# Kernel tuning notes

Measured on AMD Instinct MI355X. Metric: run time of the kernel, lower is better.

Reference implementation:

```python
import jax, jax.numpy as jnp
import numpy as np

GRID_SIZE = 5
SPLINE_ORDER = 3
NUM_BASIS = GRID_SIZE + SPLINE_ORDER  # 8
GRID = jnp.linspace(-1.0, 1.0, GRID_SIZE + 2 * SPLINE_ORDER + 1)  # [12]
EPS = 1e-6


def bspline_basis(x):
    """Iterative Cox-de Boor. x: [...]; returns [..., NUM_BASIS]."""
    xe = x[..., None]
    # order-0 indicator basis: [..., G-1]
    B = ((xe >= GRID[:-1]) & (xe < GRID[1:])).astype(x.dtype)
    for k in range(1, SPLINE_ORDER + 1):
        nb = B.shape[-1] - 1
        g_i = GRID[:nb]
        g_i1 = GRID[1:1 + nb]
        g_ik = GRID[k:k + nb]
        g_ik1 = GRID[k + 1:k + 1 + nb]
        dl = g_ik - g_i
        dr = g_ik1 - g_i1
        left = jnp.where(dl > EPS, (xe - g_i) / jnp.where(dl > EPS, dl, 1.0), 0.0) * B[..., :nb]
        right = jnp.where(dr > EPS, (g_ik1 - xe) / jnp.where(dr > EPS, dr, 1.0), 0.0) * B[..., 1:nb + 1]
        B = left + right
    return B[..., :NUM_BASIS]


def setup_inputs() -> dict:
    key = jax.random.key(0)
    k1, k2 = jax.random.split(key)
    x = jax.random.normal(k1, (8192, 512), dtype=jnp.float32)
    spline_coeffs = jax.random.normal(k2, (512, 512, NUM_BASIS), dtype=jnp.float32) * 0.1
    return {"x": x, "spline_coeffs": spline_coeffs}


def reference(x, spline_coeffs):
    xn = jnp.tanh(x)                       # [B, in]
    basis = bspline_basis(xn)              # [B, in, K]
    # output[b, o] = sum_{i,k} coeffs[o, i, k] * basis[b, i, k]
    return jnp.einsum('bik,oik->bo', basis, spline_coeffs)
```

## Files before the change

### kernel.cpp

```cpp
#include <hip/hip_runtime.h>
#include <hip/hip_bf16.h>
#include <stdint.h>


#define M_TOTAL 8192
#define N_DIM   512
#define K_DIM   4096
#define BM 128
#define BN 128
#define BK 64
#define NT_HALF 32
#define GRP_LDS 65536
#define BUF_HALF 32768

typedef __attribute__((ext_vector_type(8))) short short8;
typedef __attribute__((ext_vector_type(4))) float f32x4;

typedef const __attribute__((address_space(1))) uint32_t ga_u32;
typedef __attribute__((address_space(3))) uint32_t ls_u32;

__device__ __forceinline__ void gload_lds16(const void* g, void* l) {
  __builtin_amdgcn_global_load_lds((ga_u32*)(uintptr_t)g,
                                   (ls_u32*)(uint32_t)(uintptr_t)l, 16, 0, 0);
}

__device__ __forceinline__ uint32_t f2bf(float f) {
  uint32_t u = __builtin_bit_cast(uint32_t, f);
  return (u + 0x7FFFu + ((u >> 16) & 1u)) >> 16;
}

__device__ __forceinline__ void basis_slots(float xv, uint32_t o[4]) {
  xv = fminf(15.f, fmaxf(-15.f, xv));
  float e  = __expf(2.0f * xv);
  float t  = (e - 1.0f) * __builtin_amdgcn_rcpf(e + 1.0f);
  float uf = (t + 1.0f) * 5.5f;
  int   c  = (int)uf;  c = c > 10 ? 10 : c;
  float u  = uf - (float)c;
  float u2 = u * u, u3 = u2 * u, om = 1.0f - u;
  float w0 = om * om * om * (1.0f / 6.0f);
  float w1 = (3.0f * u3 - 6.0f * u2 + 4.0f) * (1.0f / 6.0f);
  float w2 = (-3.0f * u3 + 3.0f * u2 + 3.0f * u + 1.0f) * (1.0f / 6.0f);
  float w3 = u3 * (1.0f / 6.0f);
  uint32_t p01 = f2bf(w0) | (f2bf(w1) << 16);
  uint32_t p23 = f2bf(w2) | (f2bf(w3) << 16);
  uint64_t W = (uint64_t)p01 | ((uint64_t)p23 << 32);
  int d = c - 3;
  uint64_t lo = (d < 0) ? (W >> ((-d) * 16))
              : ((d < 4) ? (W << (d * 16)) : 0ull);
  uint64_t hi = (d <= 0) ? 0ull
              : ((d < 4) ? (W >> ((4 - d) * 16)) : (W << ((d - 4) * 16)));
  o[0] = (uint32_t)lo; o[1] = (uint32_t)(lo >> 32);
  o[2] = (uint32_t)hi; o[3] = (uint32_t)(hi >> 32);
}

__global__ __launch_bounds__(256) void basis_kernel(const float* __restrict__ x,
                                                    __hip_bfloat16* __restrict__ A,
                                                    int total) {
  int idx = blockIdx.x * 256 + threadIdx.x;
  if (idx >= total) return;
  uint32_t o[4];
  basis_slots(x[idx], o);
  reinterpret_cast<int4*>(A)[idx] = make_int4(o[0], o[1], o[2], o[3]);
}

__global__ __launch_bounds__(256) void cvt_kernel(const float* __restrict__ c,
                                                  __hip_bfloat16* __restrict__ Bt,
                                                  int total8) {
  int idx = blockIdx.x * 256 + threadIdx.x;
  if (idx >= total8) return;
  const float4* cp = reinterpret_cast<const float4*>(c) + (size_t)idx * 2;
  float4 a = cp[0], b = cp[1];
  union { unsigned short us[8]; int4 v; } pk;
  pk.us[0] = (unsigned short)f2bf(a.x); pk.us[1] = (unsigned short)f2bf(a.y);
  pk.us[2] = (unsigned short)f2bf(a.z); pk.us[3] = (unsigned short)f2bf(a.w);
  pk.us[4] = (unsigned short)f2bf(b.x); pk.us[5] = (unsigned short)f2bf(b.y);
  pk.us[6] = (unsigned short)f2bf(b.z); pk.us[7] = (unsigned short)f2bf(b.w);
  reinterpret_cast<int4*>(Bt)[idx] = pk.v;
}

__global__ __launch_bounds__(512) void gemm_kernel(
    const __hip_bfloat16* __restrict__ A,
    const __hip_bfloat16* __restrict__ Bt,
    float* __restrict__ C) {
  __shared__ char lds[2 * GRP_LDS];

  const int tid   = threadIdx.x;
  const int wid   = tid >> 6;
  const int lane  = tid & 63;
  const int quad  = lane >> 4;
  const int l16   = lane & 15;
  const int kgrp  = wid >> 2;
  const int w2    = wid & 3;
  const int waveM = w2 >> 1, waveN = w2 & 1;
  const int tg    = tid & 255;

  const int b  = blockIdx.x;
  const int q  = b >> 3;
  const int mt = (b & 7) * 8 + (q >> 2);
  const int nt = q & 3;
  const int m0 = mt * BM;
  const int n0 = nt * BN;

  char* grp = lds + kgrp * GRP_LDS;

  uint32_t aGlob[4], bGlob[4], sOff[4];
#pragma unroll
  for (int t = 0; t < 4; ++t) {
    int s = t * 256 + tg, row = s >> 3, p = s & 7, cc = p ^ (row & 7);
    sOff[t]  = (uint32_t)s * 16u;
    aGlob[t] = (uint32_t)(m0 + row) * K_DIM + (uint32_t)cc * 8u
             + (uint32_t)kgrp * 2048u;
    bGlob[t] = (uint32_t)(n0 + row) * K_DIM + (uint32_t)cc * 8u
             + (uint32_t)kgrp * 2048u;
  }

  uint32_t aOff[2][4], bOff[2][4];
#pragma unroll
  for (int kk = 0; kk < 2; ++kk) {
    int c = kk * 4 + quad;
#pragma unroll
    for (int mi = 0; mi < 4; ++mi) {
      int row = waveM * 64 + mi * 16 + l16;
      aOff[kk][mi] = (uint32_t)(row * 8 + (c ^ (row & 7))) * 16u;
    }
#pragma unroll
    for (int ni = 0; ni < 4; ++ni) {
      int row = waveN * 64 + ni * 16 + l16;
      bOff[kk][ni] = 16384u + (uint32_t)(row * 8 + (c ^ (row & 7))) * 16u;
    }
  }

  f32x4 acc[4][4];
#pragma unroll
  for (int mi = 0; mi < 4; ++mi)
#pragma unroll
    for (int ni = 0; ni < 4; ++ni)
      acc[mi][ni] = (f32x4){0.f, 0.f, 0.f, 0.f};

#pragma unroll
  for (int t = 0; t < 4; ++t) {
    gload_lds16(A + aGlob[t], grp + sOff[t]);
    gload_lds16(Bt + bGlob[t], grp + 16384 + sOff[t]);
  }

  for (int it = 0; it < NT_HALF; ++it) {
    const int cur = it & 1;
    char* bufc = grp + cur * BUF_HALF;
    __syncthreads();
    if (it + 1 < NT_HALF) {
      char* bufn = grp + (1 - cur) * BUF_HALF;
      uint32_t kt = (uint32_t)(it + 1) * BK;
#pragma unroll
      for (int t = 0; t < 4; ++t) {
        gload_lds16(A + aGlob[t] + kt, bufn + sOff[t]);
        gload_lds16(Bt + bGlob[t] + kt, bufn + 16384 + sOff[t]);
      }
    }
#pragma unroll
    for (int kk = 0; kk < 2; ++kk) {
      short8 af[4], bf[4];
#pragma unroll
      for (int mi = 0; mi < 4; ++mi)
        af[mi] = *reinterpret_cast<const short8*>(bufc + aOff[kk][mi]);
#pragma unroll
      for (int ni = 0; ni < 4; ++ni)
        bf[ni] = *reinterpret_cast<const short8*>(bufc + bOff[kk][ni]);
#pragma unroll
      for (int mi = 0; mi < 4; ++mi)
#pragma unroll
        for (int ni = 0; ni < 4; ++ni)
          acc[mi][ni] = __builtin_amdgcn_mfma_f32_16x16x32_bf16(
              af[mi], bf[ni], acc[mi][ni], 0, 0, 0);
    }
  }

  __syncthreads();
  if (kgrp == 1) {
#pragma unroll
    for (int mi = 0; mi < 4; ++mi)
#pragma unroll
      for (int ni = 0; ni < 4; ++ni) {
        int f = mi * 4 + ni;
        *reinterpret_cast<f32x4*>(lds + w2 * 16384 + f * 1024 + lane * 16) =
            acc[mi][ni];
      }
  }
  __syncthreads();
  if (kgrp == 0) {
#pragma unroll
    for (int mi = 0; mi < 4; ++mi) {
#pragma unroll
      for (int ni = 0; ni < 4; ++ni) {
        int f = mi * 4 + ni;
        f32x4 other = *reinterpret_cast<f32x4*>(
            lds + w2 * 16384 + f * 1024 + lane * 16);
        f32x4 s = acc[mi][ni] + other;
        int col = n0 + waveN * 64 + ni * 16 + l16;
#pragma unroll
        for (int r = 0; r < 4; ++r) {
          int row = m0 + waveM * 64 + mi * 16 + quad * 4 + r;
          C[(size_t)row * N_DIM + col] = s[r];
        }
      }
    }
  }
}

extern "C" void kernel_launch(void* const* d_in, const int* in_sizes, int n_in,
                              void* d_out, int out_size, void* d_ws, size_t ws_size,
                              hipStream_t stream) {
  const float* x    = (const float*)d_in[0];
  const float* coef = (const float*)d_in[1];
  float* out = (float*)d_out;

  __hip_bfloat16* Bt = (__hip_bfloat16*)d_ws;
  __hip_bfloat16* A  = (__hip_bfloat16*)((char*)d_ws + (size_t)4 * 1024 * 1024);

  const int total8 = N_DIM * K_DIM / 8;
  cvt_kernel<<<(total8 + 255) / 256, 256, 0, stream>>>(coef, Bt, total8);

  const int total = M_TOTAL * 512;
  basis_kernel<<<total / 256, 256, 0, stream>>>(x, A, total);

  gemm_kernel<<<(M_TOTAL / BM) * (N_DIM / BN), 512, 0, stream>>>(A, Bt, out);
}
```

Before: 119.8 us.

## Pre-swizzle B into MFMA fragment layout and load it directly to registers

The coefficient conversion kernel now writes B in a fragment-ordered layout, so each lane loads its bf16 MFMA operands straight from global memory into registers and B no longer goes through LDS. The GEMM tile shrinks to 128x64 with 256 threads (two waves per K-group) and launch bounds allowing two blocks per CU. The main loop is unrolled by two with explicit register double-buffering for B. This cuts LDS traffic and footprint and doubles the block count. In exchange, B fragments are re-read from global memory or L2 by every M-tile, and per-block arithmetic intensity is lower.

```diff
diff --git a/kernel.cpp b/kernel.cpp
--- a/kernel.cpp
+++ b/kernel.cpp
@@ -7,11 +7,11 @@
 #define N_DIM   512
 #define K_DIM   4096
 #define BM 128
-#define BN 128
+#define BN 64
 #define BK 64
 #define NT_HALF 32
-#define GRP_LDS 65536
-#define BUF_HALF 32768
+#define ABUF 16384
+#define GRP_LDS 32768
 
 typedef __attribute__((ext_vector_type(8))) short short8;
 typedef __attribute__((ext_vector_type(4))) float f32x4;
@@ -64,71 +64,74 @@
 }
 
 __global__ __launch_bounds__(256) void cvt_kernel(const float* __restrict__ c,
-                                                  __hip_bfloat16* __restrict__ Bt,
-                                                  int total8) {
+                                                  __hip_bfloat16* __restrict__ Btf,
+                                                  int total) {
   int idx = blockIdx.x * 256 + threadIdx.x;
-  if (idx >= total8) return;
-  const float4* cp = reinterpret_cast<const float4*>(c) + (size_t)idx * 2;
-  float4 a = cp[0], b = cp[1];
+  if (idx >= total) return;
+  int lane = idx & 63;
+  int g    = idx >> 6;
+  int ni   = g & 3;
+  int kk   = (g >> 2) & 1;
+  int it   = (g >> 3) & 31;
+  int kgrp = (g >> 8) & 1;
+  int nt   = g >> 9;
+  int n  = nt * 64 + ni * 16 + (lane & 15);
+  int k0 = kgrp * 2048 + it * 64 + kk * 32 + (lane >> 4) * 8;
+  const float4* src = reinterpret_cast<const float4*>(c + (size_t)n * K_DIM + k0);
+  float4 a = src[0], b = src[1];
   union { unsigned short us[8]; int4 v; } pk;
   pk.us[0] = (unsigned short)f2bf(a.x); pk.us[1] = (unsigned short)f2bf(a.y);
   pk.us[2] = (unsigned short)f2bf(a.z); pk.us[3] = (unsigned short)f2bf(a.w);
   pk.us[4] = (unsigned short)f2bf(b.x); pk.us[5] = (unsigned short)f2bf(b.y);
   pk.us[6] = (unsigned short)f2bf(b.z); pk.us[7] = (unsigned short)f2bf(b.w);
-  reinterpret_cast<int4*>(Bt)[idx] = pk.v;
-}
-
-__global__ __launch_bounds__(512) void gemm_kernel(
+  reinterpret_cast<int4*>(Btf)[idx] = pk.v;
+}
+
+__global__ __launch_bounds__(256, 2) void gemm_kernel(
     const __hip_bfloat16* __restrict__ A,
-    const __hip_bfloat16* __restrict__ Bt,
+    const __hip_bfloat16* __restrict__ Btf,
     float* __restrict__ C) {
   __shared__ char lds[2 * GRP_LDS];
 
-  const int tid   = threadIdx.x;
-  const int wid   = tid >> 6;
-  const int lane  = tid & 63;
-  const int quad  = lane >> 4;
-  const int l16   = lane & 15;
-  const int kgrp  = wid >> 2;
-  const int w2    = wid & 3;
-  const int waveM = w2 >> 1, waveN = w2 & 1;
-  const int tg    = tid & 255;
+  const int tid  = threadIdx.x;
+  const int lane = tid & 63;
+  const int quad = lane >> 4;
+  const int l16  = lane & 15;
+  const int kgrp = tid >> 7;
+  const int wv   = (tid >> 6) & 1;
+  const int tg   = tid & 127;
 
   const int b  = blockIdx.x;
   const int q  = b >> 3;
-  const int mt = (b & 7) * 8 + (q >> 2);
-  const int nt = q & 3;
+  const int mt = (b & 7) * 8 + (q >> 3);
+  const int nt = q & 7;
   const int m0 = mt * BM;
   const int n0 = nt * BN;
 
   char* grp = lds + kgrp * GRP_LDS;
 
-  uint32_t aGlob[4], bGlob[4], sOff[4];
-#pragma unroll
-  for (int t = 0; t < 4; ++t) {
-    int s = t * 256 + tg, row = s >> 3, p = s & 7, cc = p ^ (row & 7);
+  uint32_t aGlob[8], sOff[8];
+#pragma unroll
+  for (int t = 0; t < 8; ++t) {
+    int s = t * 128 + tg, row = s >> 3, p = s & 7, cc = p ^ (row & 7);
     sOff[t]  = (uint32_t)s * 16u;
-    aGlob[t] = (uint32_t)(m0 + row) * K_DIM + (uint32_t)cc * 8u
-             + (uint32_t)kgrp * 2048u;
-    bGlob[t] = (uint32_t)(n0 + row) * K_DIM + (uint32_t)cc * 8u
-             + (uint32_t)kgrp * 2048u;
-  }
-
-  uint32_t aOff[2][4], bOff[2][4];
+    aGlob[t] = (uint32_t)(m0 + row) * K_DIM + (uint32_t)kgrp * 2048u
+             + (uint32_t)cc * 8u;
+  }
+
+  uint32_t aOff[2][4];
 #pragma unroll
   for (int kk = 0; kk < 2; ++kk) {
     int c = kk * 4 + quad;
 #pragma unroll
     for (int mi = 0; mi < 4; ++mi) {
-      int row = waveM * 64 + mi * 16 + l16;
+      int row = wv * 64 + mi * 16 + l16;
       aOff[kk][mi] = (uint32_t)(row * 8 + (c ^ (row & 7))) * 16u;
     }
-#pragma unroll
-    for (int ni = 0; ni < 4; ++ni) {
-      int row = waveN * 64 + ni * 16 + l16;
-      bOff[kk][ni] = 16384u + (uint32_t)(row * 8 + (c ^ (row & 7))) * 16u;
-    }
-  }
+  }
+
+  const char* bBase = (const char*)Btf
+      + (size_t)(nt * 2 + kgrp) * 32 * 8192 + (size_t)lane * 16;
 
   f32x4 acc[4][4];
 #pragma unroll
@@ -137,41 +140,42 @@
     for (int ni = 0; ni < 4; ++ni)
       acc[mi][ni] = (f32x4){0.f, 0.f, 0.f, 0.f};
 
-#pragma unroll
-  for (int t = 0; t < 4; ++t) {
-    gload_lds16(A + aGlob[t], grp + sOff[t]);
-    gload_lds16(Bt + bGlob[t], grp + 16384 + sOff[t]);
-  }
-
-  for (int it = 0; it < NT_HALF; ++it) {
-    const int cur = it & 1;
-    char* bufc = grp + cur * BUF_HALF;
+  short8 b0[2][4], b1[2][4];
+
+#define STAGE_A(it, buf)                                                 \
+  { _Pragma("unroll") for (int t = 0; t < 8; ++t)                        \
+      gload_lds16(A + aGlob[t] + (uint32_t)(it) * 64u, (buf) + sOff[t]); }
+#define LOAD_B(dst, it)                                                  \
+  { _Pragma("unroll") for (int kk = 0; kk < 2; ++kk)                     \
+      _Pragma("unroll") for (int ni = 0; ni < 4; ++ni)                   \
+        dst[kk][ni] = *reinterpret_cast<const short8*>(                  \
+            bBase + (it) * 8192 + kk * 4096 + ni * 1024); }
+#define COMPUTE(buf, bR)                                                 \
+  { _Pragma("unroll") for (int kk = 0; kk < 2; ++kk) {                   \
+      short8 af[4];                                                      \
+      _Pragma("unroll") for (int mi = 0; mi < 4; ++mi)                   \
+        af[mi] = *reinterpret_cast<const short8*>((buf) + aOff[kk][mi]); \
+      _Pragma("unroll") for (int mi = 0; mi < 4; ++mi)                   \
+        _Pragma("unroll") for (int ni = 0; ni < 4; ++ni)                 \
+          acc[mi][ni] = __builtin_amdgcn_mfma_f32_16x16x32_bf16(         \
+              af[mi], bR[kk][ni], acc[mi][ni], 0, 0, 0); } }
+
+  STAGE_A(0, grp);
+  LOAD_B(b0, 0);
+
+  for (int it = 0; it < NT_HALF; it += 2) {
     __syncthreads();
     if (it + 1 < NT_HALF) {
-      char* bufn = grp + (1 - cur) * BUF_HALF;
-      uint32_t kt = (uint32_t)(it + 1) * BK;
-#pragma unroll
-      for (int t = 0; t < 4; ++t) {
-        gload_lds16(A + aGlob[t] + kt, bufn + sOff[t]);
-        gload_lds16(Bt + bGlob[t] + kt, bufn + 16384 + sOff[t]);
-      }
-    }
-#pragma unroll
-    for (int kk = 0; kk < 2; ++kk) {
-      short8 af[4], bf[4];
-#pragma unroll
-      for (int mi = 0; mi < 4; ++mi)
-        af[mi] = *reinterpret_cast<const short8*>(bufc + aOff[kk][mi]);
-#pragma unroll
-      for (int ni = 0; ni < 4; ++ni)
-        bf[ni] = *reinterpret_cast<const short8*>(bufc + bOff[kk][ni]);
-#pragma unroll
-      for (int mi = 0; mi < 4; ++mi)
-#pragma unroll
-        for (int ni = 0; ni < 4; ++ni)
-          acc[mi][ni] = __builtin_amdgcn_mfma_f32_16x16x32_bf16(
-              af[mi], bf[ni], acc[mi][ni], 0, 0, 0);
-    }
+      STAGE_A(it + 1, grp + ABUF);
+      LOAD_B(b1, it + 1);
+    }
+    COMPUTE(grp, b0);
+    __syncthreads();
+    if (it + 2 < NT_HALF) {
+      STAGE_A(it + 2, grp);
+      LOAD_B(b0, it + 2);
+    }
+    COMPUTE(grp + ABUF, b1);
   }
 
   __syncthreads();
@@ -181,7 +185,7 @@
 #pragma unroll
       for (int ni = 0; ni < 4; ++ni) {
         int f = mi * 4 + ni;
-        *reinterpret_cast<f32x4*>(lds + w2 * 16384 + f * 1024 + lane * 16) =
+        *reinterpret_cast<f32x4*>(lds + wv * 16384 + f * 1024 + lane * 16) =
             acc[mi][ni];
       }
   }
@@ -193,12 +197,12 @@
       for (int ni = 0; ni < 4; ++ni) {
         int f = mi * 4 + ni;
         f32x4 other = *reinterpret_cast<f32x4*>(
-            lds + w2 * 16384 + f * 1024 + lane * 16);
+            lds + wv * 16384 + f * 1024 + lane * 16);
         f32x4 s = acc[mi][ni] + other;
-        int col = n0 + waveN * 64 + ni * 16 + l16;
+        int col = n0 + ni * 16 + l16;
 #pragma unroll
         for (int r = 0; r < 4; ++r) {
-          int row = m0 + waveM * 64 + mi * 16 + quad * 4 + r;
+          int row = m0 + wv * 64 + mi * 16 + quad * 4 + r;
           C[(size_t)row * N_DIM + col] = s[r];
         }
       }
@@ -213,14 +217,14 @@
   const float* coef = (const float*)d_in[1];
   float* out = (float*)d_out;
 
-  __hip_bfloat16* Bt = (__hip_bfloat16*)d_ws;
-  __hip_bfloat16* A  = (__hip_bfloat16*)((char*)d_ws + (size_t)4 * 1024 * 1024);
+  __hip_bfloat16* Btf = (__hip_bfloat16*)d_ws;
+  __hip_bfloat16* A   = (__hip_bfloat16*)((char*)d_ws + (size_t)4 * 1024 * 1024);
 
   const int total8 = N_DIM * K_DIM / 8;
-  cvt_kernel<<<(total8 + 255) / 256, 256, 0, stream>>>(coef, Bt, total8);
+  cvt_kernel<<<(total8 + 255) / 256, 256, 0, stream>>>(coef, Btf, total8);
 
   const int total = M_TOTAL * 512;
   basis_kernel<<<total / 256, 256, 0, stream>>>(x, A, total);
 
-  gemm_kernel<<<(M_TOTAL / BM) * (N_DIM / BN), 512, 0, stream>>>(A, Bt, out);
-}
+  gemm_kernel<<<(M_TOTAL / BM) * (N_DIM / BN), 256, 0, stream>>>(A, Btf, out);
+}
```

Result: slower. 124.1 us (+3.6%).
